# Performance work log

Hardware: AMD Instinct MI355X
Metric: run time of the kernel (lower is better)

Reference implementation:

```python
import jax, jax.numpy as jnp
import numpy as np

HEAD_SIZE = 64  # EMBEDDING_SIZE(384) // HEAD_NO(6)

def setup_inputs() -> dict:
    key = jax.random.key(0)
    ks = jax.random.split(key, 6)
    B, T, C, H, D = 256, 256, 384, 6, 64
    s = 0.02
    return {
        "x": jax.random.normal(ks[0], (B, T, C), dtype=jnp.float32),
        "Wq": jax.random.normal(ks[1], (H, C, D), dtype=jnp.float32) * s,
        "Wk": jax.random.normal(ks[2], (H, C, D), dtype=jnp.float32) * s,
        "Wv": jax.random.normal(ks[3], (H, C, D), dtype=jnp.float32) * s,
        "Wproj": jax.random.normal(ks[4], (C, C), dtype=jnp.float32) * s,
        "bproj": jnp.zeros((C,), dtype=jnp.float32),
    }

def reference(x, Wq, Wk, Wv, Wproj, bproj):
    B, T, C = x.shape
    # per-head projections, stacked over heads h: [B, H, T, D]
    q = jnp.einsum('btc,hcd->bhtd', x, Wq)
    k = jnp.einsum('btc,hcd->bhtd', x, Wk)
    v = jnp.einsum('btc,hcd->bhtd', x, Wv)
    scale = 1.0 / jnp.sqrt(jnp.asarray(HEAD_SIZE, dtype=x.dtype))
    # scores [B, H, T, T]; causal mask (masked_fill then /scale == scale then mask, since -inf/scale=-inf)
    scores = jnp.einsum('bhtd,bhsd->bhts', q, k) * scale
    causal = jnp.tril(jnp.ones((T, T), dtype=bool))
    scores = jnp.where(causal, scores, -jnp.inf)
    w = jax.nn.softmax(scores, axis=-1)
    # dropout is identity in eval mode
    out = jnp.einsum('bhts,bhsd->bhtd', w, v)          # [B, H, T, D]
    out = out.transpose(0, 2, 1, 3).reshape(B, T, C)    # concat heads -> [B, T, C]
    return out @ Wproj + bproj
```

## Files before the change

kernel.cpp:

```cpp
#include <hip/hip_runtime.h>
#include <hip/hip_bf16.h>

typedef __bf16 bf16;
typedef unsigned int u32;
typedef __attribute__((ext_vector_type(8))) __bf16 bf16x8;
typedef __attribute__((ext_vector_type(4))) float f32x4;

#define Bsz 256
#define Tsz 256
#define Csz 384
#define Hn  6
#define Dh  64
#define NQKV 1152

#define MFMA16(a, b, c) __builtin_amdgcn_mfma_f32_16x16x32_bf16(a, b, c, 0, 0, 0)

typedef __attribute__((address_space(3))) u32 lds_u32;
typedef __attribute__((address_space(1))) const u32 gbl_u32;
__device__ __forceinline__ void gl2lds16(const void* g, void* l) {
    __builtin_amdgcn_global_load_lds((gbl_u32*)g, (lds_u32*)l, 16, 0, 0);
}

__device__ __forceinline__ float redmax16(float x) {
    x = fmaxf(x, __shfl_xor(x, 1));
    x = fmaxf(x, __shfl_xor(x, 2));
    x = fmaxf(x, __shfl_xor(x, 4));
    x = fmaxf(x, __shfl_xor(x, 8));
    return x;
}
__device__ __forceinline__ float redsum16(float x) {
    x += __shfl_xor(x, 1);
    x += __shfl_xor(x, 2);
    x += __shfl_xor(x, 4);
    x += __shfl_xor(x, 8);
    return x;
}

__global__ __launch_bounds__(256) void convert_x(
    const float* __restrict__ x, bf16* __restrict__ xb)
{
    size_t i = ((size_t)blockIdx.x * 256 + threadIdx.x) * 8;
    float4 f0 = *(const float4*)&x[i];
    float4 f1 = *(const float4*)&x[i + 4];
    bf16x8 o;
    o[0] = (bf16)f0.x; o[1] = (bf16)f0.y; o[2] = (bf16)f0.z; o[3] = (bf16)f0.w;
    o[4] = (bf16)f1.x; o[5] = (bf16)f1.y; o[6] = (bf16)f1.z; o[7] = (bf16)f1.w;
    *(bf16x8*)&xb[i] = o;
}

__global__ __launch_bounds__(384) void prep_w(
    const float* __restrict__ Wq, const float* __restrict__ Wk,
    const float* __restrict__ Wv, const float* __restrict__ Wp,
    bf16* __restrict__ Btqkv, bf16* __restrict__ Bpt)
{
    const int n = blockIdx.x, k = threadIdx.x;
    if (n < NQKV) {
        int wi = n / Csz, rem = n - wi * Csz, h = rem >> 6, d = rem & 63;
        const float* W = wi == 0 ? Wq : (wi == 1 ? Wk : Wv);
        Btqkv[(size_t)n * Csz + k] = (bf16)W[((size_t)h * Csz + k) * Dh + d];
    } else {
        int n2 = n - NQKV;
        Bpt[(size_t)n2 * Csz + k] = (bf16)Wp[(size_t)k * Csz + n2];
    }
}

__global__ __launch_bounds__(256) void qkv_gemm(
    const bf16* __restrict__ A, const bf16* __restrict__ Bt,
    bf16* __restrict__ q, bf16* __restrict__ k, bf16* __restrict__ v)
{
    __shared__ bf16 As[128][64];
    __shared__ bf16 Bs[128][64];
    const int tid = threadIdx.x, w = tid >> 6, lane = tid & 63;
    const int l4 = lane & 15, quad = lane >> 4;
    const int wm = w & 1, wn = w >> 1;
    const int m0 = blockIdx.x * 128, n0 = blockIdx.y * 128;
    const int srow = lane >> 3;
    const int skk  = (lane & 7) * 8;

    f32x4 acc[4][4] = {};

    for (int kc = 0; kc < Csz / 64; ++kc) {
        #pragma unroll
        for (int i = 0; i < 4; ++i) {
            int r = (w * 4 + i) * 8 + srow;
            gl2lds16(&A [(size_t)(m0 + r) * Csz + kc * 64 + skk],
                     (char*)&As[0][0] + (w * 4 + i) * 1024);
            gl2lds16(&Bt[(size_t)(n0 + r) * Csz + kc * 64 + skk],
                     (char*)&Bs[0][0] + (w * 4 + i) * 1024);
        }
        __syncthreads();
        #pragma unroll
        for (int ks = 0; ks < 2; ++ks) {
            bf16x8 af[4], bfr[4];
            #pragma unroll
            for (int mt = 0; mt < 4; ++mt)
                af[mt] = *(const bf16x8*)&As[wm * 64 + mt * 16 + l4][ks * 32 + quad * 8];
            #pragma unroll
            for (int nt = 0; nt < 4; ++nt)
                bfr[nt] = *(const bf16x8*)&Bs[wn * 64 + nt * 16 + l4][ks * 32 + quad * 8];
            #pragma unroll
            for (int mt = 0; mt < 4; ++mt)
                #pragma unroll
                for (int nt = 0; nt < 4; ++nt)
                    acc[mt][nt] = MFMA16(af[mt], bfr[nt], acc[mt][nt]);
        }
        __syncthreads();
    }

    #pragma unroll
    for (int nt = 0; nt < 4; ++nt) {
        int n = n0 + wn * 64 + nt * 16 + l4;
        int wi = n / Csz, rem = n - wi * Csz;
        int h = rem >> 6, d = rem & 63;
        bf16* outp = wi == 0 ? q : (wi == 1 ? k : v);
        #pragma unroll
        for (int mt = 0; mt < 4; ++mt)
            #pragma unroll
            for (int r = 0; r < 4; ++r) {
                int m = m0 + wm * 64 + mt * 16 + quad * 4 + r;
                int b = m >> 8, t = m & 255;
                outp[(((size_t)(b * Hn + h)) * Tsz + t) * Dh + d] = (bf16)acc[mt][nt][r];
            }
    }
}

__global__ __launch_bounds__(256) void attn_mfma(
    const bf16* __restrict__ q, const bf16* __restrict__ k, const bf16* __restrict__ v,
    bf16* __restrict__ att)
{
    __shared__ bf16 Kl[64][72];
    __shared__ bf16 Vt[64][72];
    __shared__ bf16 Pl[4][16][72];
    const float SCL = 0.18033688f;
    const int tid = threadIdx.x, w = tid >> 6, lane = tid & 63;
    const int l4 = lane & 15, quad = lane >> 4;
    const int blk = blockIdx.x;
    const int bh = blk >> 2, qt = blk & 3;
    const int b = bh / Hn, h = bh % Hn;
    const bf16* qb = q + (size_t)bh * Tsz * Dh;
    const bf16* kb = k + (size_t)bh * Tsz * Dh;
    const bf16* vb = v + (size_t)bh * Tsz * Dh;

    const int trow = qt * 64 + w * 16 + l4;
    const bf16x8 qa0 = *(const bf16x8*)&qb[trow * Dh + quad * 8];
    const bf16x8 qa1 = *(const bf16x8*)&qb[trow * Dh + 32 + quad * 8];

    f32x4 o[4] = {f32x4{0,0,0,0}, f32x4{0,0,0,0}, f32x4{0,0,0,0}, f32x4{0,0,0,0}};
    float mrun[4] = {-3.0e38f, -3.0e38f, -3.0e38f, -3.0e38f};
    float lrun[4] = {0.f, 0.f, 0.f, 0.f};

    for (int kt = 0; kt <= qt; ++kt) {
        #pragma unroll
        for (int it = 0; it < 2; ++it) {
            int idx = it * 256 + tid;
            int s = idx >> 3, d8 = (idx & 7) * 8;
            *(bf16x8*)&Kl[s][d8] = *(const bf16x8*)&kb[(kt * 64 + s) * Dh + d8];
        }
        #pragma unroll
        for (int it = 0; it < 2; ++it) {
            int idx = it * 256 + tid;
            int s = idx & 63, d8 = (idx >> 6) * 8;
            bf16x8 vv = *(const bf16x8*)&vb[(kt * 64 + s) * Dh + d8];
            #pragma unroll
            for (int j = 0; j < 8; ++j) Vt[d8 + j][s] = vv[j];
        }
        __syncthreads();

        f32x4 sc[4] = {f32x4{0,0,0,0}, f32x4{0,0,0,0}, f32x4{0,0,0,0}, f32x4{0,0,0,0}};
        #pragma unroll
        for (int nt = 0; nt < 4; ++nt) {
            bf16x8 b0 = *(const bf16x8*)&Kl[nt * 16 + l4][quad * 8];
            bf16x8 b1 = *(const bf16x8*)&Kl[nt * 16 + l4][32 + quad * 8];
            sc[nt] = MFMA16(qa0, b0, sc[nt]);
            sc[nt] = MFMA16(qa1, b1, sc[nt]);
        }

        float mnew[4], alpha[4];
        #pragma unroll
        for (int r = 0; r < 4; ++r) {
            int tg = qt * 64 + w * 16 + quad * 4 + r;
            float mx = mrun[r];
            #pragma unroll
            for (int nt = 0; nt < 4; ++nt) {
                float sv = sc[nt][r] * SCL;
                int sg = kt * 64 + nt * 16 + l4;
                if (sg > tg) sv = -1.0e30f;
                sc[nt][r] = sv;
                mx = fmaxf(mx, sv);
            }
            mx = redmax16(mx);
            mnew[r] = mx;
            alpha[r] = __builtin_amdgcn_exp2f(mrun[r] - mx);
            mrun[r] = mx;
        }
        #pragma unroll
        for (int r = 0; r < 4; ++r) {
            float sm = 0.f;
            #pragma unroll
            for (int nt = 0; nt < 4; ++nt) {
                float e = __builtin_amdgcn_exp2f(sc[nt][r] - mnew[r]);
                sc[nt][r] = e;
                sm += e;
            }
            sm = redsum16(sm);
            lrun[r] = lrun[r] * alpha[r] + sm;
        }
        #pragma unroll
        for (int nt = 0; nt < 4; ++nt)
            #pragma unroll
            for (int r = 0; r < 4; ++r) o[nt][r] *= alpha[r];

        #pragma unroll
        for (int nt = 0; nt < 4; ++nt)
            #pragma unroll
            for (int r = 0; r < 4; ++r)
                Pl[w][quad * 4 + r][nt * 16 + l4] = (bf16)sc[nt][r];

        bf16x8 pa0 = *(const bf16x8*)&Pl[w][l4][quad * 8];
        bf16x8 pa1 = *(const bf16x8*)&Pl[w][l4][32 + quad * 8];
        #pragma unroll
        for (int nt = 0; nt < 4; ++nt) {
            bf16x8 vb0 = *(const bf16x8*)&Vt[nt * 16 + l4][quad * 8];
            bf16x8 vb1 = *(const bf16x8*)&Vt[nt * 16 + l4][32 + quad * 8];
            o[nt] = MFMA16(pa0, vb0, o[nt]);
            o[nt] = MFMA16(pa1, vb1, o[nt]);
        }
        __syncthreads();
    }

    #pragma unroll
    for (int r = 0; r < 4; ++r) {
        float inv = 1.f / lrun[r];
        int tg = qt * 64 + w * 16 + quad * 4 + r;
        #pragma unroll
        for (int nt = 0; nt < 4; ++nt)
            att[((size_t)(b * Tsz + tg)) * Csz + h * Dh + nt * 16 + l4] =
                (bf16)(o[nt][r] * inv);
    }
}

__global__ __launch_bounds__(256) void proj_gemm(
    const bf16* __restrict__ A, const bf16* __restrict__ Bt,
    const float* __restrict__ bias, float* __restrict__ out)
{
    __shared__ bf16 As[128][64];
    __shared__ bf16 Bs[128][64];
    const int tid = threadIdx.x, w = tid >> 6, lane = tid & 63;
    const int l4 = lane & 15, quad = lane >> 4;
    const int wm = w & 1, wn = w >> 1;
    const int m0 = blockIdx.x * 128, n0 = blockIdx.y * 128;
    const int srow = lane >> 3;
    const int skk  = (lane & 7) * 8;

    f32x4 acc[4][4] = {};

    for (int kc = 0; kc < Csz / 64; ++kc) {
        #pragma unroll
        for (int i = 0; i < 4; ++i) {
            int r = (w * 4 + i) * 8 + srow;
            gl2lds16(&A [(size_t)(m0 + r) * Csz + kc * 64 + skk],
                     (char*)&As[0][0] + (w * 4 + i) * 1024);
            gl2lds16(&Bt[(size_t)(n0 + r) * Csz + kc * 64 + skk],
                     (char*)&Bs[0][0] + (w * 4 + i) * 1024);
        }
        __syncthreads();
        #pragma unroll
        for (int ks = 0; ks < 2; ++ks) {
            bf16x8 af[4], bfr[4];
            #pragma unroll
            for (int mt = 0; mt < 4; ++mt)
                af[mt] = *(const bf16x8*)&As[wm * 64 + mt * 16 + l4][ks * 32 + quad * 8];
            #pragma unroll
            for (int nt = 0; nt < 4; ++nt)
                bfr[nt] = *(const bf16x8*)&Bs[wn * 64 + nt * 16 + l4][ks * 32 + quad * 8];
            #pragma unroll
            for (int mt = 0; mt < 4; ++mt)
                #pragma unroll
                for (int nt = 0; nt < 4; ++nt)
                    acc[mt][nt] = MFMA16(af[mt], bfr[nt], acc[mt][nt]);
        }
        __syncthreads();
    }

    #pragma unroll
    for (int nt = 0; nt < 4; ++nt) {
        int n = n0 + wn * 64 + nt * 16 + l4;
        float bv = bias[n];
        #pragma unroll
        for (int mt = 0; mt < 4; ++mt)
            #pragma unroll
            for (int r = 0; r < 4; ++r) {
                int m = m0 + wm * 64 + mt * 16 + quad * 4 + r;
                out[(size_t)m * Csz + n] = acc[mt][nt][r] + bv;
            }
    }
}

extern "C" void kernel_launch(void* const* d_in, const int* in_sizes, int n_in,
                              void* d_out, int out_size, void* d_ws, size_t ws_size,
                              hipStream_t stream)
{
    const float* x  = (const float*)d_in[0];
    const float* Wq = (const float*)d_in[1];
    const float* Wk = (const float*)d_in[2];
    const float* Wv = (const float*)d_in[3];
    const float* Wp = (const float*)d_in[4];
    const float* bp = (const float*)d_in[5];
    float* out = (float*)d_out;

    const size_t npe = (size_t)Bsz * Tsz * Csz;
    bf16* xb    = (bf16*)d_ws;
    bf16* att   = xb;
    bf16* q     = xb + npe;
    bf16* k     = q  + npe;
    bf16* v     = k  + npe;
    bf16* Btqkv = v  + npe;
    bf16* Bpt   = Btqkv + (size_t)NQKV * Csz;

    convert_x<<<npe / 2048, 256, 0, stream>>>(x, xb);
    prep_w<<<NQKV + Csz, 384, 0, stream>>>(Wq, Wk, Wv, Wp, Btqkv, Bpt);
    qkv_gemm<<<dim3(Bsz * Tsz / 128, NQKV / 128), 256, 0, stream>>>(xb, Btqkv, q, k, v);
    attn_mfma<<<Bsz * Hn * 4, 256, 0, stream>>>(q, k, v, att);
    proj_gemm<<<dim3(Bsz * Tsz / 128, Csz / 128), 256, 0, stream>>>(att, Bpt, bp, out);
}
```

Measured before the change: 435.4 us.

## Triple-buffer GEMMs with swizzled LDS, larger tiles, and XCD-aware block remapping

Both GEMMs move to 256x128 tiles with a three-stage LDS ring loaded through global_load_lds. Partial vmcnt waits let the next tiles stream in while the current one computes, and an XOR swizzle is meant to cut LDS bank conflicts. Block indices in the GEMMs and in attention are remapped so that neighbouring tiles land on the same XCD for L2 reuse, and s_setprio is raised around the MFMA bursts. In exchange, the 144KB LDS footprint limits occupancy to one block per CU, and the larger accumulators raise register pressure.

```diff
diff --git a/kernel.cpp b/kernel.cpp
--- a/kernel.cpp
+++ b/kernel.cpp
@@ -64,62 +64,145 @@
     }
 }
 
-__global__ __launch_bounds__(256) void qkv_gemm(
+
+__device__ __forceinline__ void stage_tile(
+    const char* Ab, const char* Bb, int m0, int n0, int t,
+    bf16 (*As)[256][64], bf16 (*Bs)[128][64], int buf, int tid)
+{
+    const int srow = tid >> 3;
+    const int scs  = ((tid & 7) * 16) ^ (((tid >> 3) & 7) << 4);
+    #pragma unroll
+    for (int j = 0; j < 8; ++j)
+        gl2lds16(Ab + (size_t)(m0 + j * 32 + srow) * 768 + t * 128 + scs,
+                 (char*)&As[buf][0][0] + j * 4096 + tid * 16);
+    #pragma unroll
+    for (int j = 0; j < 4; ++j)
+        gl2lds16(Bb + (size_t)(n0 + j * 32 + srow) * 768 + t * 128 + scs,
+                 (char*)&Bs[buf][0][0] + j * 4096 + tid * 16);
+}
+
+__device__ __forceinline__ void compute_tile(
+    const bf16 (*As)[256][64], const bf16 (*Bs)[128][64], int buf,
+    int wmw, int wnw, int l4, int quad, f32x4 acc[8][4])
+{
+    const char* Ap = (const char*)&As[buf][0][0];
+    const char* Bp = (const char*)&Bs[buf][0][0];
+    const int cswz = (l4 & 7) << 4;
+    bf16x8 bfr[4][2];
+    #pragma unroll
+    for (int fn = 0; fn < 4; ++fn)
+        #pragma unroll
+        for (int ks = 0; ks < 2; ++ks)
+            bfr[fn][ks] = *(const bf16x8*)(Bp + (wnw * 64 + fn * 16 + l4) * 128 +
+                                           ((ks * 64 + quad * 16) ^ cswz));
+    #pragma unroll
+    for (int mh = 0; mh < 2; ++mh) {
+        bf16x8 af[4][2];
+        #pragma unroll
+        for (int fr = 0; fr < 4; ++fr)
+            #pragma unroll
+            for (int ks = 0; ks < 2; ++ks)
+                af[fr][ks] = *(const bf16x8*)(Ap + (wmw * 128 + mh * 64 + fr * 16 + l4) * 128 +
+                                              ((ks * 64 + quad * 16) ^ cswz));
+        __builtin_amdgcn_s_setprio(1);
+        #pragma unroll
+        for (int ks = 0; ks < 2; ++ks)
+            #pragma unroll
+            for (int fr = 0; fr < 4; ++fr)
+                #pragma unroll
+                for (int fn = 0; fn < 4; ++fn)
+                    acc[mh * 4 + fr][fn] = MFMA16(af[fr][ks], bfr[fn][ks], acc[mh * 4 + fr][fn]);
+        __builtin_amdgcn_s_setprio(0);
+    }
+}
+
+#define GEMM_PIPE()                                                            \
+    stage_tile(Ab, Bb, m0, n0, 0, As, Bs, 0, tid);                             \
+    stage_tile(Ab, Bb, m0, n0, 1, As, Bs, 1, tid);                             \
+    asm volatile("s_waitcnt vmcnt(12)" ::: "memory");                          \
+    __builtin_amdgcn_s_barrier();                                              \
+    _Pragma("unroll")                                                          \
+    for (int t = 0; t < 6; ++t) {                                              \
+        if (t < 4) stage_tile(Ab, Bb, m0, n0, t + 2, As, Bs, (t + 2) % 3, tid);\
+        compute_tile(As, Bs, t % 3, wmw, wnw, l4, quad, acc);                  \
+        if (t < 4) {                                                           \
+            asm volatile("s_waitcnt vmcnt(12)" ::: "memory");                  \
+            __builtin_amdgcn_s_barrier();                                      \
+        } else if (t == 4) {                                                   \
+            asm volatile("s_waitcnt vmcnt(0)" ::: "memory");                   \
+            __builtin_amdgcn_s_barrier();                                      \
+        }                                                                      \
+    }
+
+__global__ __launch_bounds__(256, 1) void qkv_gemm(
     const bf16* __restrict__ A, const bf16* __restrict__ Bt,
     bf16* __restrict__ q, bf16* __restrict__ k, bf16* __restrict__ v)
 {
-    __shared__ bf16 As[128][64];
-    __shared__ bf16 Bs[128][64];
+    __shared__ bf16 As[3][256][64];
+    __shared__ bf16 Bs[3][128][64];
     const int tid = threadIdx.x, w = tid >> 6, lane = tid & 63;
     const int l4 = lane & 15, quad = lane >> 4;
-    const int wm = w & 1, wn = w >> 1;
-    const int m0 = blockIdx.x * 128, n0 = blockIdx.y * 128;
-    const int srow = lane >> 3;
-    const int skk  = (lane & 7) * 8;
-
-    f32x4 acc[4][4] = {};
-
-    for (int kc = 0; kc < Csz / 64; ++kc) {
-        #pragma unroll
-        for (int i = 0; i < 4; ++i) {
-            int r = (w * 4 + i) * 8 + srow;
-            gl2lds16(&A [(size_t)(m0 + r) * Csz + kc * 64 + skk],
-                     (char*)&As[0][0] + (w * 4 + i) * 1024);
-            gl2lds16(&Bt[(size_t)(n0 + r) * Csz + kc * 64 + skk],
-                     (char*)&Bs[0][0] + (w * 4 + i) * 1024);
-        }
-        __syncthreads();
-        #pragma unroll
-        for (int ks = 0; ks < 2; ++ks) {
-            bf16x8 af[4], bfr[4];
-            #pragma unroll
-            for (int mt = 0; mt < 4; ++mt)
-                af[mt] = *(const bf16x8*)&As[wm * 64 + mt * 16 + l4][ks * 32 + quad * 8];
-            #pragma unroll
-            for (int nt = 0; nt < 4; ++nt)
-                bfr[nt] = *(const bf16x8*)&Bs[wn * 64 + nt * 16 + l4][ks * 32 + quad * 8];
-            #pragma unroll
-            for (int mt = 0; mt < 4; ++mt)
-                #pragma unroll
-                for (int nt = 0; nt < 4; ++nt)
-                    acc[mt][nt] = MFMA16(af[mt], bfr[nt], acc[mt][nt]);
-        }
-        __syncthreads();
-    }
-
-    #pragma unroll
-    for (int nt = 0; nt < 4; ++nt) {
-        int n = n0 + wn * 64 + nt * 16 + l4;
+    const int wmw = w >> 1, wnw = w & 1;
+
+    const int orig = blockIdx.x;
+    const int id = (orig & 7) * 288 + (orig >> 3);
+    const int mt_ = id / 9, nt_ = id - mt_ * 9;
+    const int m0 = mt_ * 256, n0 = nt_ * 128;
+
+    const char* Ab = (const char*)A;
+    const char* Bb = (const char*)Bt;
+    f32x4 acc[8][4] = {};
+
+    GEMM_PIPE();
+
+    #pragma unroll
+    for (int fn = 0; fn < 4; ++fn) {
+        int n = n0 + wnw * 64 + fn * 16 + l4;
         int wi = n / Csz, rem = n - wi * Csz;
         int h = rem >> 6, d = rem & 63;
         bf16* outp = wi == 0 ? q : (wi == 1 ? k : v);
         #pragma unroll
-        for (int mt = 0; mt < 4; ++mt)
+        for (int fr = 0; fr < 8; ++fr)
             #pragma unroll
             for (int r = 0; r < 4; ++r) {
-                int m = m0 + wm * 64 + mt * 16 + quad * 4 + r;
-                int b = m >> 8, t = m & 255;
-                outp[(((size_t)(b * Hn + h)) * Tsz + t) * Dh + d] = (bf16)acc[mt][nt][r];
+                int m = m0 + wmw * 128 + fr * 16 + quad * 4 + r;
+                int b = m >> 8, tt = m & 255;
+                outp[(((size_t)(b * Hn + h)) * Tsz + tt) * Dh + d] = (bf16)acc[fr][fn][r];
+            }
+    }
+}
+
+__global__ __launch_bounds__(256, 1) void proj_gemm(
+    const bf16* __restrict__ A, const bf16* __restrict__ Bt,
+    const float* __restrict__ bias, float* __restrict__ out)
+{
+    __shared__ bf16 As[3][256][64];
+    __shared__ bf16 Bs[3][128][64];
+    const int tid = threadIdx.x, w = tid >> 6, lane = tid & 63;
+    const int l4 = lane & 15, quad = lane >> 4;
+    const int wmw = w >> 1, wnw = w & 1;
+
+    const int orig = blockIdx.x;
+    const int id = (orig & 7) * 96 + (orig >> 3);
+    const int mt_ = id / 3, nt_ = id - mt_ * 3;
+    const int m0 = mt_ * 256, n0 = nt_ * 128;
+
+    const char* Ab = (const char*)A;
+    const char* Bb = (const char*)Bt;
+    f32x4 acc[8][4] = {};
+
+    GEMM_PIPE();
+
+    #pragma unroll
+    for (int fn = 0; fn < 4; ++fn) {
+        int n = n0 + wnw * 64 + fn * 16 + l4;
+        float bv = bias[n];
+        #pragma unroll
+        for (int fr = 0; fr < 8; ++fr)
+            #pragma unroll
+            for (int r = 0; r < 4; ++r) {
+                int m = m0 + wmw * 128 + fr * 16 + quad * 4 + r;
+                out[(size_t)m * Csz + n] = acc[fr][fn][r] + bv;
             }
     }
 }
@@ -134,7 +217,9 @@
     const float SCL = 0.18033688f;
     const int tid = threadIdx.x, w = tid >> 6, lane = tid & 63;
     const int l4 = lane & 15, quad = lane >> 4;
-    const int blk = blockIdx.x;
+
+    const int orig = blockIdx.x;
+    const int blk = (orig & 7) * 768 + (orig >> 3);
     const int bh = blk >> 2, qt = blk & 3;
     const int b = bh / Hn, h = bh % Hn;
     const bf16* qb = q + (size_t)bh * Tsz * Dh;
@@ -239,63 +324,6 @@
     }
 }
 
-__global__ __launch_bounds__(256) void proj_gemm(
-    const bf16* __restrict__ A, const bf16* __restrict__ Bt,
-    const float* __restrict__ bias, float* __restrict__ out)
-{
-    __shared__ bf16 As[128][64];
-    __shared__ bf16 Bs[128][64];
-    const int tid = threadIdx.x, w = tid >> 6, lane = tid & 63;
-    const int l4 = lane & 15, quad = lane >> 4;
-    const int wm = w & 1, wn = w >> 1;
-    const int m0 = blockIdx.x * 128, n0 = blockIdx.y * 128;
-    const int srow = lane >> 3;
-    const int skk  = (lane & 7) * 8;
-
-    f32x4 acc[4][4] = {};
-
-    for (int kc = 0; kc < Csz / 64; ++kc) {
-        #pragma unroll
-        for (int i = 0; i < 4; ++i) {
-            int r = (w * 4 + i) * 8 + srow;
-            gl2lds16(&A [(size_t)(m0 + r) * Csz + kc * 64 + skk],
-                     (char*)&As[0][0] + (w * 4 + i) * 1024);
-            gl2lds16(&Bt[(size_t)(n0 + r) * Csz + kc * 64 + skk],
-                     (char*)&Bs[0][0] + (w * 4 + i) * 1024);
-        }
-        __syncthreads();
-        #pragma unroll
-        for (int ks = 0; ks < 2; ++ks) {
-            bf16x8 af[4], bfr[4];
-            #pragma unroll
-            for (int mt = 0; mt < 4; ++mt)
-                af[mt] = *(const bf16x8*)&As[wm * 64 + mt * 16 + l4][ks * 32 + quad * 8];
-            #pragma unroll
-            for (int nt = 0; nt < 4; ++nt)
-                bfr[nt] = *(const bf16x8*)&Bs[wn * 64 + nt * 16 + l4][ks * 32 + quad * 8];
-            #pragma unroll
-            for (int mt = 0; mt < 4; ++mt)
-                #pragma unroll
-                for (int nt = 0; nt < 4; ++nt)
-                    acc[mt][nt] = MFMA16(af[mt], bfr[nt], acc[mt][nt]);
-        }
-        __syncthreads();
-    }
-
-    #pragma unroll
-    for (int nt = 0; nt < 4; ++nt) {
-        int n = n0 + wn * 64 + nt * 16 + l4;
-        float bv = bias[n];
-        #pragma unroll
-        for (int mt = 0; mt < 4; ++mt)
-            #pragma unroll
-            for (int r = 0; r < 4; ++r) {
-                int m = m0 + wm * 64 + mt * 16 + quad * 4 + r;
-                out[(size_t)m * Csz + n] = acc[mt][nt][r] + bv;
-            }
-    }
-}
-
 extern "C" void kernel_launch(void* const* d_in, const int* in_sizes, int n_in,
                               void* d_out, int out_size, void* d_ws, size_t ws_size,
                               hipStream_t stream)
@@ -319,7 +347,7 @@
 
     convert_x<<<npe / 2048, 256, 0, stream>>>(x, xb);
     prep_w<<<NQKV + Csz, 384, 0, stream>>>(Wq, Wk, Wv, Wp, Btqkv, Bpt);
-    qkv_gemm<<<dim3(Bsz * Tsz / 128, NQKV / 128), 256, 0, stream>>>(xb, Btqkv, q, k, v);
+    qkv_gemm<<<(Bsz * Tsz / 256) * (NQKV / 128), 256, 0, stream>>>(xb, Btqkv, q, k, v);
     attn_mfma<<<Bsz * Hn * 4, 256, 0, stream>>>(q, k, v, att);
-    proj_gemm<<<dim3(Bsz * Tsz / 128, Csz / 128), 256, 0, stream>>>(att, Bpt, bp, out);
-}
+    proj_gemm<<<(Bsz * Tsz / 256) * (Csz / 128), 256, 0, stream>>>(att, Bpt, bp, out);
+}
```

New measurement: 387.5 us. 1.12x faster.
